# Performance work log

Hardware: AMD Instinct MI355X
Metric: run time of the kernel (lower is better)

The kernel has to match this reference:

```python
import jax, jax.numpy as jnp
import numpy as np

# config constants
H = 2048          # hidden_size
I_MOE = 1408      # moe_intermediate_size
E = 8             # n_routed_experts
TOP_K = 2         # num_experts_per_tok
NG = 4            # n_group
TOPK_G = 2        # topk_group
SCALE = 2.5       # routed_scaling_factor
N_SHARED = 2      # n_shared_experts
I_SHARED = I_MOE * N_SHARED
B, S = 1, 2048


def setup_inputs() -> dict:
    key = jax.random.key(0)
    ks = jax.random.split(key, 9)
    sc = 0.02
    return {
        "x": jax.random.normal(ks[0], (B, S, H), dtype=jnp.float32),
        "router_weight": jax.random.normal(ks[1], (E, H), dtype=jnp.float32) * sc,
        "e_score_correction_bias": jnp.zeros((E,), dtype=jnp.float32),
        "gate_w": jax.random.normal(ks[2], (E, I_MOE, H), dtype=jnp.float32) * sc,
        "up_w": jax.random.normal(ks[3], (E, I_MOE, H), dtype=jnp.float32) * sc,
        "down_w": jax.random.normal(ks[4], (E, H, I_MOE), dtype=jnp.float32) * sc,
        "shared_gate_w": jax.random.normal(ks[5], (I_SHARED, H), dtype=jnp.float32) * sc,
        "shared_up_w": jax.random.normal(ks[6], (I_SHARED, H), dtype=jnp.float32) * sc,
        "shared_down_w": jax.random.normal(ks[7], (H, I_SHARED), dtype=jnp.float32) * sc,
    }


def _mlp(x, gw, uw, dw):
    # SwiGLU MLP: down( silu(gate(x)) * up(x) )
    return (jax.nn.silu(x @ gw.T) * (x @ uw.T)) @ dw.T


def _route(x2d, rw, bias):
    T = x2d.shape[0]
    logits = x2d.astype(jnp.float32) @ rw.astype(jnp.float32).T          # [T,E]
    scores = jax.nn.sigmoid(logits)                                       # [T,E]
    sfc = scores + bias[None, :]                                          # [T,E]
    # group scores: sum of top-2 per group
    grp = sfc.reshape(T, NG, E // NG)
    group_scores = jnp.sum(jax.lax.top_k(grp, 2)[0], axis=-1)             # [T,NG]
    grp_idx = jax.lax.top_k(group_scores, TOPK_G)[1]                      # [T,topk_group]
    group_mask = jnp.zeros((T, NG), jnp.float32).at[
        jnp.arange(T)[:, None], grp_idx].set(1.0)                         # [T,NG]
    score_mask = jnp.repeat(group_mask, E // NG, axis=1)                  # [T,E]
    masked = jnp.where(score_mask > 0, sfc, 0.0)
    topk_idx = jax.lax.top_k(masked, TOP_K)[1]                            # [T,K]
    topk_w = jnp.take_along_axis(scores, topk_idx, axis=1)                # [T,K]
    topk_w = topk_w / (jnp.sum(topk_w, axis=-1, keepdims=True) + 1e-20)   # norm_topk_prob
    return topk_idx, topk_w * SCALE


def reference(x, router_weight, e_score_correction_bias, gate_w, up_w, down_w,
              shared_gate_w, shared_up_w, shared_down_w):
    orig_shape = x.shape
    x2d = x.reshape(-1, H)                                                # [T,H]
    T = x2d.shape[0]
    topk_idx, topk_w = _route(x2d, router_weight, e_score_correction_bias)
    # per-token per-expert combine weights [T,E] (top-k indices are distinct per token)
    cw = jnp.zeros((T, E), jnp.float32).at[
        jnp.arange(T)[:, None], topk_idx].add(topk_w)

    def expert_body(acc, ws):
        gw, uw, dw, cwe = ws  # gw/uw:[I,H], dw:[H,I], cwe:[T]
        y = _mlp(x2d, gw, uw, dw)
        return acc + cwe[:, None] * y, None

    routed, _ = jax.lax.scan(expert_body, jnp.zeros_like(x2d),
                             (gate_w, up_w, down_w, cw.T))
    out = routed.reshape(orig_shape) + _mlp(x, shared_gate_w, shared_up_w, shared_down_w)
    return out
```

## Files before the change

kernel.cpp:

```cpp
#include <hip/hip_runtime.h>
#include <hip/hip_bf16.h>
#include <math.h>

#define H 2048
#define IMOE 1408
#define NEXP 8
#define T_TOK 2048
#define ISH 2816
#define SCALEF 2.5f

#define NT_GU_R (IMOE / 64)
#define NT_GU_S (ISH / 64)
#define NT_DN   (H / 128)
#define GU_GRID (39 * NT_GU_R + 16 * NT_GU_S)
#define DN_GRID (39 * NT_DN + 16 * NT_DN)

typedef __attribute__((ext_vector_type(8))) short short8;
typedef __attribute__((ext_vector_type(4))) short short4v;
typedef __attribute__((ext_vector_type(4))) float floatx4;

union U8 { short8 s; unsigned u[4]; };

__device__ inline float b2f(short v) {
    unsigned int u = ((unsigned int)(unsigned short)v) << 16;
    float f; __builtin_memcpy(&f, &u, 4); return f;
}
__device__ inline short f2b(float f) {
    __hip_bfloat16 h = __float2bfloat16(f);
    short s; __builtin_memcpy(&s, &h, 2); return s;
}
__device__ __forceinline__ unsigned pkbf16(float a, float b) {
    float2 t; t.x = a; t.y = b;
    __hip_bfloat162 h2 = __float22bfloat162_rn(t);
    unsigned u; __builtin_memcpy(&u, &h2, 4); return u;
}

__device__ __forceinline__ void async16(const short* g, short* l) {
    __builtin_amdgcn_global_load_lds(
        (const __attribute__((address_space(1))) unsigned*)g,
        (__attribute__((address_space(3))) unsigned*)l, 16, 0, 0);
}
__device__ __forceinline__ void async16f(const float* g, float* l) {
    __builtin_amdgcn_global_load_lds(
        (const __attribute__((address_space(1))) unsigned*)g,
        (__attribute__((address_space(3))) unsigned*)l, 16, 0, 0);
}

__device__ __forceinline__ int xcd_map(int orig, int nwg) {
    int q = nwg >> 3, r = nwg & 7;
    int x = orig & 7, s = orig >> 3;
    int base = (x < r) ? x * (q + 1) : r * (q + 1) + (x - r) * q;
    return base + s;
}

__global__ __launch_bounds__(256) void router_kernel(
    const float* __restrict__ x, const float* __restrict__ rw,
    const float* __restrict__ bias,
    int* __restrict__ cnt, int* __restrict__ tokList, int* __restrict__ slotList,
    float* __restrict__ pairW, short* __restrict__ xb)
{
    const int wid  = (blockIdx.x * 256 + threadIdx.x) >> 6;
    const int lane = threadIdx.x & 63;
    if (wid >= T_TOK) return;
    const float* xr = x + (size_t)wid * H;
    short* xbrow = xb + (size_t)wid * H;

    float acc[NEXP];
#pragma unroll
    for (int e = 0; e < NEXP; ++e) acc[e] = 0.f;

#pragma unroll
    for (int c = 0; c < 8; ++c) {
        int idx = (c * 64 + lane) * 4;
        floatx4 xv = *(const floatx4*)(xr + idx);
#pragma unroll
        for (int e = 0; e < NEXP; ++e) {
            floatx4 wv = *(const floatx4*)(rw + e * H + idx);
            acc[e] += xv.x * wv.x + xv.y * wv.y + xv.z * wv.z + xv.w * wv.w;
        }
        short4v o = { f2b(xv.x), f2b(xv.y), f2b(xv.z), f2b(xv.w) };
        *(short4v*)(xbrow + idx) = o;
    }
#pragma unroll
    for (int e = 0; e < NEXP; ++e)
        for (int off = 32; off; off >>= 1)
            acc[e] += __shfl_xor(acc[e], off, 64);

    if (lane == 0) {
        float s[NEXP], sfc[NEXP];
#pragma unroll
        for (int e = 0; e < NEXP; ++e) {
            s[e]   = 1.0f / (1.0f + expf(-acc[e]));
            sfc[e] = s[e] + bias[e];
        }
        float gs[4];
#pragma unroll
        for (int g = 0; g < 4; ++g) gs[g] = sfc[2 * g] + sfc[2 * g + 1];
        int g1 = 0;
        for (int g = 1; g < 4; ++g) if (gs[g] > gs[g1]) g1 = g;
        int g2 = -1;
        for (int g = 0; g < 4; ++g) {
            if (g == g1) continue;
            if (g2 < 0 || gs[g] > gs[g2]) g2 = g;
        }
        float msk[NEXP];
#pragma unroll
        for (int e = 0; e < NEXP; ++e) {
            int g = e >> 1;
            msk[e] = (g == g1 || g == g2) ? sfc[e] : 0.0f;
        }
        int e1 = 0;
        for (int e = 1; e < NEXP; ++e) if (msk[e] > msk[e1]) e1 = e;
        int e2 = -1;
        for (int e = 0; e < NEXP; ++e) {
            if (e == e1) continue;
            if (e2 < 0 || msk[e] > msk[e2]) e2 = e;
        }
        float w1 = s[e1], w2 = s[e2];
        float inv = SCALEF / (w1 + w2 + 1e-20f);
        w1 *= inv; w2 *= inv;
        int p1 = atomicAdd(&cnt[e1], 1);
        tokList[e1 * T_TOK + p1]  = wid;
        slotList[e1 * T_TOK + p1] = 2 * wid;
        pairW[2 * wid] = w1;
        int p2 = atomicAdd(&cnt[e2], 1);
        tokList[e2 * T_TOK + p2]  = wid;
        slotList[e2 * T_TOK + p2] = 2 * wid + 1;
        pairW[2 * wid + 1] = w2;
    }
}

__global__ void plan_kernel(const int* __restrict__ cnt, int* __restrict__ meta)
{
    if (blockIdx.x != 0 || threadIdx.x != 0) return;
    int base = 0, gu = 0, dn = 0;
    meta[20] = 0; meta[32] = 0;
    for (int e = 0; e < NEXP; ++e) {
        int M = cnt[e];
        meta[e] = M;
        meta[9 + e] = base;
        base += M;
        int MT = (M + 127) >> 7;
        gu += MT * NT_GU_R;
        dn += MT * NT_DN;
        meta[21 + e] = gu;
        meta[33 + e] = dn;
    }
    meta[8]  = T_TOK;
    meta[17] = 0;
    meta[29] = gu + 16 * NT_GU_S;
    meta[41] = dn + 16 * NT_DN;
}

__global__ __launch_bounds__(256) void gu_gemm(
    const short* __restrict__ xb,
    const float* __restrict__ gw, const float* __restrict__ uw,
    const float* __restrict__ sgw, const float* __restrict__ suw,
    short* __restrict__ hiddenP, short* __restrict__ hiddenS,
    const int* __restrict__ tokList, const int* __restrict__ meta)
{
    const int total = meta[29];
    if (blockIdx.x >= total) return;
    const int idx = xcd_map(blockIdx.x, total);
    int e = 0;
    while (e < 8 && idx >= meta[21 + e]) ++e;

    int M, NT, Nout, rowBase;
    const float *b1, *b2;
    const int* gat;
    short* outP;
    if (e < 8) {
        M = meta[e]; NT = NT_GU_R; Nout = IMOE; rowBase = meta[9 + e];
        b1 = gw + (size_t)e * IMOE * H;
        b2 = uw + (size_t)e * IMOE * H;
        gat = tokList + e * T_TOK;
        outP = hiddenP;
    } else {
        M = T_TOK; NT = NT_GU_S; Nout = ISH; rowBase = 0;
        b1 = sgw; b2 = suw; gat = nullptr; outP = hiddenS;
    }
    const int MT = (M + 127) >> 7;
    const int local = idx - meta[20 + e];
    const int mt = local % MT;
    const int nt = local / MT;

    __shared__ short As[128 * 64];
    __shared__ float Bg[64 * 64];
    __shared__ float Bu[64 * 64];

    const int tid  = threadIdx.x;
    const int w    = tid >> 6;
    const int lane = tid & 63;
    const int quad = lane >> 4;
    const int l16  = lane & 15;
    const int wm = w >> 1, wn = w & 1;

    const int r8 = lane >> 3;
    const int csA = (lane & 7) ^ r8;
    const short* aSrc[4];
    short* ldsA[4];
#pragma unroll
    for (int i = 0; i < 4; ++i) {
        int r = w * 32 + i * 8 + r8;
        int p = mt * 128 + r;
        int pos = p < M ? p : (M - 1);
        int arow = gat ? gat[pos] : pos;
        aSrc[i] = xb + (size_t)arow * H + csA * 8;
        ldsA[i] = As + (w * 32 + i * 8) * 64;
    }

    const int br4 = lane >> 4;
    const int bc  = lane & 15;
    const float* bgSrc[4];
    const float* buSrc[4];
    float* ldsBg[4];
    float* ldsBu[4];
#pragma unroll
    for (int i = 0; i < 4; ++i) {
        int rb = w * 16 + i * 4;
        int row = rb + br4;
        int sc = bc ^ (row & 15);
        bgSrc[i] = b1 + (size_t)(nt * 64 + row) * H + sc * 4;
        buSrc[i] = b2 + (size_t)(nt * 64 + row) * H + sc * 4;
        ldsBg[i] = Bg + rb * 64;
        ldsBu[i] = Bu + rb * 64;
    }

    floatx4 accg[4][2] = {};
    floatx4 accu[4][2] = {};

    for (int k0 = 0; k0 < H; k0 += 64) {
#pragma unroll
        for (int i = 0; i < 4; ++i) async16(aSrc[i] + k0, ldsA[i]);
#pragma unroll
        for (int i = 0; i < 4; ++i) async16f(bgSrc[i] + k0, ldsBg[i]);
#pragma unroll
        for (int i = 0; i < 4; ++i) async16f(buSrc[i] + k0, ldsBu[i]);
        __syncthreads();

        const int sw = l16 & 7;
        short8 af[4], bgf[2], buf[2];
#pragma unroll
        for (int kk2 = 0; kk2 < 2; ++kk2) {
            const int c = kk2 * 4 + quad;
#pragma unroll
            for (int m = 0; m < 4; ++m)
                af[m] = *(const short8*)(As + (wm * 64 + m * 16 + l16) * 64 + (c ^ sw) * 8);
#pragma unroll
            for (int n = 0; n < 2; ++n) {
                int rg = wn * 32 + n * 16 + l16;
                const float* pg = Bg + rg * 64;
                const float* pu = Bu + rg * 64;
                int j0 = ((2 * c)     ^ (rg & 15)) * 4;
                int j1 = ((2 * c + 1) ^ (rg & 15)) * 4;
                floatx4 g0 = *(const floatx4*)(pg + j0);
                floatx4 g1 = *(const floatx4*)(pg + j1);
                floatx4 u0 = *(const floatx4*)(pu + j0);
                floatx4 u1 = *(const floatx4*)(pu + j1);
                U8 tg, tu;
                tg.u[0] = pkbf16(g0.x, g0.y); tg.u[1] = pkbf16(g0.z, g0.w);
                tg.u[2] = pkbf16(g1.x, g1.y); tg.u[3] = pkbf16(g1.z, g1.w);
                tu.u[0] = pkbf16(u0.x, u0.y); tu.u[1] = pkbf16(u0.z, u0.w);
                tu.u[2] = pkbf16(u1.x, u1.y); tu.u[3] = pkbf16(u1.z, u1.w);
                bgf[n] = tg.s;
                buf[n] = tu.s;
            }
#pragma unroll
            for (int m = 0; m < 4; ++m)
#pragma unroll
                for (int n = 0; n < 2; ++n) {
                    accg[m][n] = __builtin_amdgcn_mfma_f32_16x16x32_bf16(af[m], bgf[n], accg[m][n], 0, 0, 0);
                    accu[m][n] = __builtin_amdgcn_mfma_f32_16x16x32_bf16(af[m], buf[n], accu[m][n], 0, 0, 0);
                }
        }
        __syncthreads();
    }

#pragma unroll
    for (int m = 0; m < 4; ++m) {
#pragma unroll
        for (int rr = 0; rr < 4; ++rr) {
            int lr = wm * 64 + m * 16 + quad * 4 + rr;
            int p = mt * 128 + lr;
            if (p >= M) continue;
            size_t rowoff = (size_t)(rowBase + p) * Nout + nt * 64 + wn * 32;
#pragma unroll
            for (int n = 0; n < 2; ++n) {
                float g = accg[m][n][rr];
                float u = accu[m][n][rr];
                outP[rowoff + n * 16 + l16] = f2b(g / (1.0f + __expf(-g)) * u);
            }
        }
    }
}

__global__ __launch_bounds__(256) void dn_gemm(
    const short* __restrict__ hiddenP, const short* __restrict__ hiddenS,
    const float* __restrict__ dw, const float* __restrict__ sdw,
    short* __restrict__ outPairs, short* __restrict__ sharedOut,
    const int* __restrict__ slotList, const int* __restrict__ meta)
{
    const int total = meta[41];
    if (blockIdx.x >= total) return;
    const int rtot = meta[40];
    int idx;
    if (blockIdx.x < rtot) idx = xcd_map(blockIdx.x, rtot);
    else                   idx = rtot + xcd_map(blockIdx.x - rtot, total - rtot);
    int e = 0;
    while (e < 8 && idx >= meta[33 + e]) ++e;

    int M, K, rowBase;
    const float* bp;
    const short* Abase;
    const int* scat;
    short* outP;
    if (e < 8) {
        M = meta[e]; K = IMOE; rowBase = meta[9 + e];
        bp = dw + (size_t)e * H * IMOE;
        Abase = hiddenP; scat = slotList + e * T_TOK; outP = outPairs;
    } else {
        M = T_TOK; K = ISH; rowBase = 0;
        bp = sdw; Abase = hiddenS; scat = nullptr; outP = sharedOut;
    }
    const int MT = (M + 127) >> 7;
    const int local = idx - meta[32 + e];
    const int mt = local % MT;
    const int nt = local / MT;

    __shared__ short As[128 * 64];
    __shared__ float Bf[128 * 64];

    const int tid  = threadIdx.x;
    const int w    = tid >> 6;
    const int lane = tid & 63;
    const int quad = lane >> 4;
    const int l16  = lane & 15;
    const int wm = w >> 1, wn = w & 1;

    const int r8 = lane >> 3;
    const int csA = (lane & 7) ^ r8;
    const short* aSrc[4];
    short* ldsA[4];
#pragma unroll
    for (int i = 0; i < 4; ++i) {
        int r = w * 32 + i * 8 + r8;
        int p = mt * 128 + r;
        int pos = p < M ? p : (M - 1);
        aSrc[i] = Abase + (size_t)(rowBase + pos) * K + csA * 8;
        ldsA[i] = As + (w * 32 + i * 8) * 64;
    }

    const int br4 = lane >> 4;
    const int bc  = lane & 15;
    const float* bSrc[8];
    float* ldsB[8];
#pragma unroll
    for (int i = 0; i < 8; ++i) {
        int rb = w * 32 + i * 4;
        int row = rb + br4;
        int sc = bc ^ (row & 15);
        bSrc[i] = bp + (size_t)(nt * 128 + row) * K + sc * 4;
        ldsB[i] = Bf + rb * 64;
    }

    floatx4 acc[4][4] = {};

    const int kIters = K >> 6;
    for (int kt = 0; kt < kIters; ++kt) {
        const int k0 = kt << 6;
#pragma unroll
        for (int i = 0; i < 4; ++i) async16(aSrc[i] + k0, ldsA[i]);
#pragma unroll
        for (int i = 0; i < 8; ++i) async16f(bSrc[i] + k0, ldsB[i]);
        __syncthreads();

        const int sw = l16 & 7;
        short8 af[4], bf[4];
#pragma unroll
        for (int kk2 = 0; kk2 < 2; ++kk2) {
            const int c = kk2 * 4 + quad;
#pragma unroll
            for (int m = 0; m < 4; ++m)
                af[m] = *(const short8*)(As + (wm * 64 + m * 16 + l16) * 64 + (c ^ sw) * 8);
#pragma unroll
            for (int n = 0; n < 4; ++n) {
                int rb2 = wn * 64 + n * 16 + l16;
                const float* pb = Bf + rb2 * 64;
                floatx4 b0 = *(const floatx4*)(pb + (((2 * c)     ^ (rb2 & 15)) * 4));
                floatx4 b1 = *(const floatx4*)(pb + (((2 * c + 1) ^ (rb2 & 15)) * 4));
                U8 t;
                t.u[0] = pkbf16(b0.x, b0.y); t.u[1] = pkbf16(b0.z, b0.w);
                t.u[2] = pkbf16(b1.x, b1.y); t.u[3] = pkbf16(b1.z, b1.w);
                bf[n] = t.s;
            }
#pragma unroll
            for (int m = 0; m < 4; ++m)
#pragma unroll
                for (int n = 0; n < 4; ++n)
                    acc[m][n] = __builtin_amdgcn_mfma_f32_16x16x32_bf16(af[m], bf[n], acc[m][n], 0, 0, 0);
        }
        __syncthreads();
    }

#pragma unroll
    for (int m = 0; m < 4; ++m) {
#pragma unroll
        for (int rr = 0; rr < 4; ++rr) {
            int lr = wm * 64 + m * 16 + quad * 4 + rr;
            int p = mt * 128 + lr;
            if (p >= M) continue;
            int crow = scat ? scat[p] : p;
            size_t rowoff = (size_t)crow * H + nt * 128 + wn * 64;
#pragma unroll
            for (int n = 0; n < 4; ++n)
                outP[rowoff + n * 16 + l16] = f2b(acc[m][n][rr]);
        }
    }
}

__global__ __launch_bounds__(256) void combine_kernel(
    const short* __restrict__ outPairs, const short* __restrict__ sharedOut,
    const float* __restrict__ pairW, float* __restrict__ out)
{
    size_t gi = ((size_t)blockIdx.x * 256 + threadIdx.x) * 8;
    int t = (int)(gi >> 11);
    int h = (int)(gi & (H - 1));
    float w0 = pairW[2 * t], w1 = pairW[2 * t + 1];
    short8 p0 = *(const short8*)(outPairs + (size_t)(2 * t) * H + h);
    short8 p1 = *(const short8*)(outPairs + (size_t)(2 * t + 1) * H + h);
    short8 sh = *(const short8*)(sharedOut + gi);
    floatx4 o0, o1;
#pragma unroll
    for (int j = 0; j < 4; ++j)
        o0[j] = w0 * b2f(p0[j]) + w1 * b2f(p1[j]) + b2f(sh[j]);
#pragma unroll
    for (int j = 0; j < 4; ++j)
        o1[j] = w0 * b2f(p0[4 + j]) + w1 * b2f(p1[4 + j]) + b2f(sh[4 + j]);
    *(floatx4*)(out + gi)     = o0;
    *(floatx4*)(out + gi + 4) = o1;
}

extern "C" void kernel_launch(void* const* d_in, const int* in_sizes, int n_in,
                              void* d_out, int out_size, void* d_ws, size_t ws_size,
                              hipStream_t stream)
{
    const float* x    = (const float*)d_in[0];
    const float* rw   = (const float*)d_in[1];
    const float* bias = (const float*)d_in[2];
    const float* gw   = (const float*)d_in[3];
    const float* uw   = (const float*)d_in[4];
    const float* dw   = (const float*)d_in[5];
    const float* sgw  = (const float*)d_in[6];
    const float* suw  = (const float*)d_in[7];
    const float* sdw  = (const float*)d_in[8];
    float* out = (float*)d_out;

    char* ws = (char*)d_ws;
    size_t off = 0;
    auto alloc = [&](size_t bytes) {
        off = (off + 255) & ~(size_t)255;
        void* p = ws + off;
        off += bytes;
        return p;
    };
    int*   cnt       = (int*)  alloc(NEXP * sizeof(int));
    int*   tokList   = (int*)  alloc((size_t)NEXP * T_TOK * sizeof(int));
    int*   slotList  = (int*)  alloc((size_t)NEXP * T_TOK * sizeof(int));
    float* pairW     = (float*)alloc((size_t)2 * T_TOK * sizeof(float));
    int*   meta      = (int*)  alloc(64 * sizeof(int));
    short* xb        = (short*)alloc((size_t)T_TOK * H * sizeof(short));
    short* hiddenP   = (short*)alloc((size_t)2 * T_TOK * IMOE * sizeof(short));
    short* hiddenS   = (short*)alloc((size_t)T_TOK * ISH * sizeof(short));
    short* outPairs  = (short*)alloc((size_t)2 * T_TOK * H * sizeof(short));
    short* sharedOut = (short*)alloc((size_t)T_TOK * H * sizeof(short));
    (void)ws_size;

    hipMemsetAsync(cnt, 0, NEXP * sizeof(int), stream);

    router_kernel<<<T_TOK / 4, 256, 0, stream>>>(x, rw, bias, cnt, tokList, slotList, pairW, xb);
    plan_kernel<<<1, 64, 0, stream>>>(cnt, meta);

    gu_gemm<<<GU_GRID, 256, 0, stream>>>(xb, gw, uw, sgw, suw,
                                         hiddenP, hiddenS, tokList, meta);
    dn_gemm<<<DN_GRID, 256, 0, stream>>>(hiddenP, hiddenS, dw, sdw,
                                         outPairs, sharedOut, slotList, meta);

    combine_kernel<<<(T_TOK * H / 8) / 256, 256, 0, stream>>>(outPairs, sharedOut, pairW, out);
}
```

Baseline: 622.9 us.

## Double-buffer GEMM tiles and convert weights to bf16 once at LDS store

Both the gate/up and the down GEMM kernels now double-buffer their shared-memory tiles. The next k-tile of activations is fetched with async global-to-LDS copies, and the fp32 weight tile is loaded into registers while MFMAs run on the current tile. Weights are converted to bf16 once when written to LDS, instead of being re-read as fp32 and re-packed by every wave for every fragment. This cuts LDS traffic and conversion ALU work and removes one barrier per iteration. In exchange it doubles the LDS buffers and raises register pressure from holding the staged weights.

```diff
diff --git a/kernel.cpp b/kernel.cpp
--- a/kernel.cpp
+++ b/kernel.cpp
@@ -14,6 +14,7 @@
 #define NT_DN   (H / 128)
 #define GU_GRID (39 * NT_GU_R + 16 * NT_GU_S)
 #define DN_GRID (39 * NT_DN + 16 * NT_DN)
+#define LHALF 8192
 
 typedef __attribute__((ext_vector_type(8))) short short8;
 typedef __attribute__((ext_vector_type(4))) short short4v;
@@ -36,11 +37,6 @@
 }
 
 __device__ __forceinline__ void async16(const short* g, short* l) {
-    __builtin_amdgcn_global_load_lds(
-        (const __attribute__((address_space(1))) unsigned*)g,
-        (__attribute__((address_space(3))) unsigned*)l, 16, 0, 0);
-}
-__device__ __forceinline__ void async16f(const float* g, float* l) {
     __builtin_amdgcn_global_load_lds(
         (const __attribute__((address_space(1))) unsigned*)g,
         (__attribute__((address_space(3))) unsigned*)l, 16, 0, 0);
@@ -184,9 +180,8 @@
     const int mt = local % MT;
     const int nt = local / MT;
 
-    __shared__ short As[128 * 64];
-    __shared__ float Bg[64 * 64];
-    __shared__ float Bu[64 * 64];
+    __shared__ short As[2 * LHALF];
+    __shared__ short Bgu[2 * LHALF];
 
     const int tid  = threadIdx.x;
     const int w    = tid >> 6;
@@ -209,35 +204,60 @@
         ldsA[i] = As + (w * 32 + i * 8) * 64;
     }
 
-    const int br4 = lane >> 4;
-    const int bc  = lane & 15;
-    const float* bgSrc[4];
-    const float* buSrc[4];
-    float* ldsBg[4];
-    float* ldsBu[4];
-#pragma unroll
-    for (int i = 0; i < 4; ++i) {
-        int rb = w * 16 + i * 4;
-        int row = rb + br4;
-        int sc = bc ^ (row & 15);
-        bgSrc[i] = b1 + (size_t)(nt * 64 + row) * H + sc * 4;
-        buSrc[i] = b2 + (size_t)(nt * 64 + row) * H + sc * 4;
-        ldsBg[i] = Bg + rb * 64;
-        ldsBu[i] = Bu + rb * 64;
-    }
+    const int brow  = tid >> 1;
+    const int bhalf = tid & 1;
+    const float* bsrc = ((brow < 64) ? (b1 + (size_t)(nt * 64 + brow) * H)
+                                     : (b2 + (size_t)(nt * 64 + brow - 64) * H))
+                        + bhalf * 32;
+    int bDstOff[4];
+#pragma unroll
+    for (int j = 0; j < 4; ++j)
+        bDstOff[j] = brow * 64 + (((bhalf * 4 + j) ^ (brow & 7)) * 8);
 
     floatx4 accg[4][2] = {};
     floatx4 accu[4][2] = {};
 
+    {
+        floatx4 breg[8];
+#pragma unroll
+        for (int j = 0; j < 4; ++j) {
+            breg[2 * j]     = *(const floatx4*)(bsrc + j * 8);
+            breg[2 * j + 1] = *(const floatx4*)(bsrc + j * 8 + 4);
+        }
+#pragma unroll
+        for (int i = 0; i < 4; ++i) async16(aSrc[i], ldsA[i]);
+#pragma unroll
+        for (int j = 0; j < 4; ++j) {
+            U8 t;
+            t.u[0] = pkbf16(breg[2*j].x,   breg[2*j].y);
+            t.u[1] = pkbf16(breg[2*j].z,   breg[2*j].w);
+            t.u[2] = pkbf16(breg[2*j+1].x, breg[2*j+1].y);
+            t.u[3] = pkbf16(breg[2*j+1].z, breg[2*j+1].w);
+            *(short8*)(Bgu + bDstOff[j]) = t.s;
+        }
+        asm volatile("s_waitcnt vmcnt(0) lgkmcnt(0)" ::: "memory");
+        __builtin_amdgcn_s_barrier();
+    }
+
+    int cur = 0;
     for (int k0 = 0; k0 < H; k0 += 64) {
-#pragma unroll
-        for (int i = 0; i < 4; ++i) async16(aSrc[i] + k0, ldsA[i]);
-#pragma unroll
-        for (int i = 0; i < 4; ++i) async16f(bgSrc[i] + k0, ldsBg[i]);
-#pragma unroll
-        for (int i = 0; i < 4; ++i) async16f(buSrc[i] + k0, ldsBu[i]);
-        __syncthreads();
-
+        const int nk = k0 + 64;
+        const int has_next = (nk < H);
+        const int noff = (cur ^ 1) * LHALF;
+
+        floatx4 breg[8];
+        if (has_next) {
+#pragma unroll
+            for (int j = 0; j < 4; ++j) {
+                breg[2 * j]     = *(const floatx4*)(bsrc + nk + j * 8);
+                breg[2 * j + 1] = *(const floatx4*)(bsrc + nk + j * 8 + 4);
+            }
+#pragma unroll
+            for (int i = 0; i < 4; ++i) async16(aSrc[i] + nk, ldsA[i] + noff);
+        }
+
+        const short* Ab = As  + cur * LHALF;
+        const short* Bb = Bgu + cur * LHALF;
         const int sw = l16 & 7;
         short8 af[4], bgf[2], buf[2];
 #pragma unroll
@@ -245,25 +265,11 @@
             const int c = kk2 * 4 + quad;
 #pragma unroll
             for (int m = 0; m < 4; ++m)
-                af[m] = *(const short8*)(As + (wm * 64 + m * 16 + l16) * 64 + (c ^ sw) * 8);
+                af[m] = *(const short8*)(Ab + (wm * 64 + m * 16 + l16) * 64 + (c ^ sw) * 8);
 #pragma unroll
             for (int n = 0; n < 2; ++n) {
-                int rg = wn * 32 + n * 16 + l16;
-                const float* pg = Bg + rg * 64;
-                const float* pu = Bu + rg * 64;
-                int j0 = ((2 * c)     ^ (rg & 15)) * 4;
-                int j1 = ((2 * c + 1) ^ (rg & 15)) * 4;
-                floatx4 g0 = *(const floatx4*)(pg + j0);
-                floatx4 g1 = *(const floatx4*)(pg + j1);
-                floatx4 u0 = *(const floatx4*)(pu + j0);
-                floatx4 u1 = *(const floatx4*)(pu + j1);
-                U8 tg, tu;
-                tg.u[0] = pkbf16(g0.x, g0.y); tg.u[1] = pkbf16(g0.z, g0.w);
-                tg.u[2] = pkbf16(g1.x, g1.y); tg.u[3] = pkbf16(g1.z, g1.w);
-                tu.u[0] = pkbf16(u0.x, u0.y); tu.u[1] = pkbf16(u0.z, u0.w);
-                tu.u[2] = pkbf16(u1.x, u1.y); tu.u[3] = pkbf16(u1.z, u1.w);
-                bgf[n] = tg.s;
-                buf[n] = tu.s;
+                bgf[n] = *(const short8*)(Bb + (wn * 32 + n * 16 + l16) * 64 + (c ^ sw) * 8);
+                buf[n] = *(const short8*)(Bb + (64 + wn * 32 + n * 16 + l16) * 64 + (c ^ sw) * 8);
             }
 #pragma unroll
             for (int m = 0; m < 4; ++m)
@@ -273,7 +279,21 @@
                     accu[m][n] = __builtin_amdgcn_mfma_f32_16x16x32_bf16(af[m], buf[n], accu[m][n], 0, 0, 0);
                 }
         }
-        __syncthreads();
+
+        if (has_next) {
+#pragma unroll
+            for (int j = 0; j < 4; ++j) {
+                U8 t;
+                t.u[0] = pkbf16(breg[2*j].x,   breg[2*j].y);
+                t.u[1] = pkbf16(breg[2*j].z,   breg[2*j].w);
+                t.u[2] = pkbf16(breg[2*j+1].x, breg[2*j+1].y);
+                t.u[3] = pkbf16(breg[2*j+1].z, breg[2*j+1].w);
+                *(short8*)(Bgu + noff + bDstOff[j]) = t.s;
+            }
+        }
+        asm volatile("s_waitcnt vmcnt(0) lgkmcnt(0)" ::: "memory");
+        __builtin_amdgcn_s_barrier();
+        cur ^= 1;
     }
 
 #pragma unroll
@@ -327,8 +347,8 @@
     const int mt = local % MT;
     const int nt = local / MT;
 
-    __shared__ short As[128 * 64];
-    __shared__ float Bf[128 * 64];
+    __shared__ short As[2 * LHALF];
+    __shared__ short Bs[2 * LHALF];
 
     const int tid  = threadIdx.x;
     const int w    = tid >> 6;
@@ -350,30 +370,58 @@
         ldsA[i] = As + (w * 32 + i * 8) * 64;
     }
 
-    const int br4 = lane >> 4;
-    const int bc  = lane & 15;
-    const float* bSrc[8];
-    float* ldsB[8];
-#pragma unroll
-    for (int i = 0; i < 8; ++i) {
-        int rb = w * 32 + i * 4;
-        int row = rb + br4;
-        int sc = bc ^ (row & 15);
-        bSrc[i] = bp + (size_t)(nt * 128 + row) * K + sc * 4;
-        ldsB[i] = Bf + rb * 64;
-    }
+    const int brow  = tid >> 1;
+    const int bhalf = tid & 1;
+    const float* bsrc = bp + (size_t)(nt * 128 + brow) * K + bhalf * 32;
+    int bDstOff[4];
+#pragma unroll
+    for (int j = 0; j < 4; ++j)
+        bDstOff[j] = brow * 64 + (((bhalf * 4 + j) ^ (brow & 7)) * 8);
 
     floatx4 acc[4][4] = {};
 
+    {
+        floatx4 breg[8];
+#pragma unroll
+        for (int j = 0; j < 4; ++j) {
+            breg[2 * j]     = *(const floatx4*)(bsrc + j * 8);
+            breg[2 * j + 1] = *(const floatx4*)(bsrc + j * 8 + 4);
+        }
+#pragma unroll
+        for (int i = 0; i < 4; ++i) async16(aSrc[i], ldsA[i]);
+#pragma unroll
+        for (int j = 0; j < 4; ++j) {
+            U8 t;
+            t.u[0] = pkbf16(breg[2*j].x,   breg[2*j].y);
+            t.u[1] = pkbf16(breg[2*j].z,   breg[2*j].w);
+            t.u[2] = pkbf16(breg[2*j+1].x, breg[2*j+1].y);
+            t.u[3] = pkbf16(breg[2*j+1].z, breg[2*j+1].w);
+            *(short8*)(Bs + bDstOff[j]) = t.s;
+        }
+        asm volatile("s_waitcnt vmcnt(0) lgkmcnt(0)" ::: "memory");
+        __builtin_amdgcn_s_barrier();
+    }
+
     const int kIters = K >> 6;
+    int cur = 0;
     for (int kt = 0; kt < kIters; ++kt) {
-        const int k0 = kt << 6;
-#pragma unroll
-        for (int i = 0; i < 4; ++i) async16(aSrc[i] + k0, ldsA[i]);
-#pragma unroll
-        for (int i = 0; i < 8; ++i) async16f(bSrc[i] + k0, ldsB[i]);
-        __syncthreads();
-
+        const int nk = (kt + 1) << 6;
+        const int has_next = (kt + 1 < kIters);
+        const int noff = (cur ^ 1) * LHALF;
+
+        floatx4 breg[8];
+        if (has_next) {
+#pragma unroll
+            for (int j = 0; j < 4; ++j) {
+                breg[2 * j]     = *(const floatx4*)(bsrc + nk + j * 8);
+                breg[2 * j + 1] = *(const floatx4*)(bsrc + nk + j * 8 + 4);
+            }
+#pragma unroll
+            for (int i = 0; i < 4; ++i) async16(aSrc[i] + nk, ldsA[i] + noff);
+        }
+
+        const short* Ab = As + cur * LHALF;
+        const short* Bb = Bs + cur * LHALF;
         const int sw = l16 & 7;
         short8 af[4], bf[4];
 #pragma unroll
@@ -381,25 +429,31 @@
             const int c = kk2 * 4 + quad;
 #pragma unroll
             for (int m = 0; m < 4; ++m)
-                af[m] = *(const short8*)(As + (wm * 64 + m * 16 + l16) * 64 + (c ^ sw) * 8);
-#pragma unroll
-            for (int n = 0; n < 4; ++n) {
-                int rb2 = wn * 64 + n * 16 + l16;
-                const float* pb = Bf + rb2 * 64;
-                floatx4 b0 = *(const floatx4*)(pb + (((2 * c)     ^ (rb2 & 15)) * 4));
-                floatx4 b1 = *(const floatx4*)(pb + (((2 * c + 1) ^ (rb2 & 15)) * 4));
-                U8 t;
-                t.u[0] = pkbf16(b0.x, b0.y); t.u[1] = pkbf16(b0.z, b0.w);
-                t.u[2] = pkbf16(b1.x, b1.y); t.u[3] = pkbf16(b1.z, b1.w);
-                bf[n] = t.s;
-            }
+                af[m] = *(const short8*)(Ab + (wm * 64 + m * 16 + l16) * 64 + (c ^ sw) * 8);
+#pragma unroll
+            for (int n = 0; n < 4; ++n)
+                bf[n] = *(const short8*)(Bb + (wn * 64 + n * 16 + l16) * 64 + (c ^ sw) * 8);
 #pragma unroll
             for (int m = 0; m < 4; ++m)
 #pragma unroll
                 for (int n = 0; n < 4; ++n)
                     acc[m][n] = __builtin_amdgcn_mfma_f32_16x16x32_bf16(af[m], bf[n], acc[m][n], 0, 0, 0);
         }
-        __syncthreads();
+
+        if (has_next) {
+#pragma unroll
+            for (int j = 0; j < 4; ++j) {
+                U8 t;
+                t.u[0] = pkbf16(breg[2*j].x,   breg[2*j].y);
+                t.u[1] = pkbf16(breg[2*j].z,   breg[2*j].w);
+                t.u[2] = pkbf16(breg[2*j+1].x, breg[2*j+1].y);
+                t.u[3] = pkbf16(breg[2*j+1].z, breg[2*j+1].w);
+                *(short8*)(Bs + noff + bDstOff[j]) = t.s;
+            }
+        }
+        asm volatile("s_waitcnt vmcnt(0) lgkmcnt(0)" ::: "memory");
+        __builtin_amdgcn_s_barrier();
+        cur ^= 1;
     }
 
 #pragma unroll
```

Result: slower. 774.5 us (+24.3%).
